# Kernel optimization log

Measured on AMD Instinct MI355X. Metric: run time of the kernel, lower is better.

The kernel has to match this reference:

```python
import jax, jax.numpy as jnp
import numpy as np

HIDDEN = 512
N_STEPS = 24
BATCH = 64
SEQ = 512
LN_EPS = 1e-5


def setup_inputs() -> dict:
    key = jax.random.key(0)
    ks = jax.random.split(key, 12)
    h = HIDDEN
    s = 0.05
    return {
        "enc_outputs": jax.random.normal(ks[0], (BATCH, SEQ, h), jnp.float32),
        "h_prev": jax.random.normal(ks[1], (1, BATCH, h), jnp.float32),
        # additive attention: score = v^T tanh(W_a [dec; enc] + b_a)
        "attn_We": jax.random.normal(ks[2], (h, h), jnp.float32) * s,   # enc half of W_a
        "attn_Wd": jax.random.normal(ks[3], (h, h), jnp.float32) * s,   # dec half of W_a
        "attn_b": jnp.zeros((h,), jnp.float32),
        "attn_v": jax.random.normal(ks[4], (h,), jnp.float32) * s,
        # GRU (PyTorch layout): W_ih (3h, 2h), W_hh (3h, h), gate order r,z,n
        "W_ih": jax.random.normal(ks[5], (3 * h, 2 * h), jnp.float32) * s,
        "W_hh": jax.random.normal(ks[6], (3 * h, h), jnp.float32) * s,
        "b_ih": jnp.zeros((3 * h,), jnp.float32),
        "b_hh": jnp.zeros((3 * h,), jnp.float32),
        # head: LayerNorm -> Linear(h, h//2) -> ReLU -> Linear(h//2, 1)
        "ln_g": jnp.ones((h,), jnp.float32),
        "ln_b": jnp.zeros((h,), jnp.float32),
        "W1": jax.random.normal(ks[7], (h, h // 2), jnp.float32) * s,
        "b1": jnp.zeros((h // 2,), jnp.float32),
        "W2": jax.random.normal(ks[8], (h // 2, 1), jnp.float32) * s,
        "b2": jnp.zeros((1,), jnp.float32),
    }


def _decode(enc_outputs, h0, attn_We, attn_Wd, attn_b, attn_v,
            W_ih, W_hh, b_ih, b_hh, ln_g, ln_b, W1, b1, W2, b2):
    H = enc_outputs.shape[-1]
    # encoder projection is loop-invariant: precompute once
    enc_proj = jnp.einsum("bse,eh->bsh", enc_outputs, attn_We)  # (B,S,H)

    def step(h, _):
        # h: (B, H) decoder state
        # additive attention
        q = h @ attn_Wd + attn_b                                  # (B,H)
        scores = jnp.einsum("bsh,h->bs", jnp.tanh(enc_proj + q[:, None, :]), attn_v)
        alpha = jax.nn.softmax(scores, axis=-1)                   # (B,S)
        context = jnp.einsum("bs,bsh->bh", alpha, enc_outputs)   # (B,H)
        # GRU cell on [context; state]
        x = jnp.concatenate([context, h], axis=-1)                # (B,2H)
        gi = x @ W_ih.T + b_ih                                    # (B,3H)
        gh = h @ W_hh.T + b_hh                                    # (B,3H)
        ir, iz, inn = jnp.split(gi, 3, axis=-1)
        hr, hz, hn = jnp.split(gh, 3, axis=-1)
        r = jax.nn.sigmoid(ir + hr)
        z = jax.nn.sigmoid(iz + hz)
        n = jnp.tanh(inn + r * hn)
        h_new = (1.0 - z) * n + z * h
        # head: LN -> Linear -> ReLU -> Linear
        mu = jnp.mean(h_new, axis=-1, keepdims=True)
        var = jnp.var(h_new, axis=-1, keepdims=True)
        y = (h_new - mu) * jax.lax.rsqrt(var + LN_EPS) * ln_g + ln_b
        y = jax.nn.relu(y @ W1 + b1)
        p = (y @ W2 + b2)[:, 0]                                   # (B,)
        return h_new, p

    h_final, preds = jax.lax.scan(step, h0, None, length=N_STEPS)
    preds = jnp.transpose(preds, (1, 0))[:, :, None]              # (B, n_steps, 1)
    return preds, h_final[None]                                   # (1,B,H)


def reference(enc_outputs, h_prev, attn_We, attn_Wd, attn_b, attn_v,
              W_ih, W_hh, b_ih, b_hh, ln_g, ln_b, W1, b1, W2, b2):
    return _decode(enc_outputs, h_prev[0], attn_We, attn_Wd, attn_b, attn_v,
                   W_ih, W_hh, b_ih, b_hh, ln_g, ln_b, W1, b1, W2, b2)
```

## Files before the change

### kernel.cpp

```cpp
#include <hip/hip_runtime.h>

typedef unsigned short u16;
typedef __attribute__((ext_vector_type(8))) short short8;
typedef __attribute__((ext_vector_type(4))) short short4v;
typedef __attribute__((ext_vector_type(4))) float f32x4;

#define NSTEP 24

__device__ __forceinline__ float b2f(u16 u){ return __uint_as_float(((unsigned)u)<<16); }
__device__ __forceinline__ u16 f2b(float f){
  unsigned u = __float_as_uint(f);
  u += 0x7fffu + ((u>>16)&1u);
  return (u16)(u>>16);
}
__device__ __forceinline__ float tanh_fast(float x){
  x = fminf(12.f, fmaxf(-12.f, x));
  float e = __expf(2.f*x);
  return __fdividef(e-1.f, e+1.f);
}
__device__ __forceinline__ float sigmoid_fast(float x){
  return __fdividef(1.f, 1.f + __expf(-x));
}

__global__ __launch_bounds__(256) void k_cvt(const float* __restrict__ in, u16* __restrict__ out, int n){
  int i = (blockIdx.x*256 + threadIdx.x)*4;
  if (i >= n) return;
  float4 v = *(const float4*)(in + i);
  short4v o;
  o[0] = (short)f2b(v.x); o[1] = (short)f2b(v.y); o[2] = (short)f2b(v.z); o[3] = (short)f2b(v.w);
  *(short4v*)(out + i) = o;
}

__global__ __launch_bounds__(256) void k_transpose512(const float* __restrict__ in, u16* __restrict__ out){
  __shared__ float tile[32][33];
  int tx = threadIdx.x, ty = threadIdx.y;
  int x = blockIdx.x*32 + tx;
  #pragma unroll
  for (int j=0;j<4;++j){
    int y = blockIdx.y*32 + ty + j*8;
    tile[ty+j*8][tx] = in[y*512 + x];
  }
  __syncthreads();
  int x2 = blockIdx.y*32 + tx;
  #pragma unroll
  for (int j=0;j<4;++j){
    int y2 = blockIdx.x*32 + ty + j*8;
    out[y2*512 + x2] = f2b(tile[tx][ty+j*8]);
  }
}

__global__ __launch_bounds__(256) void k_init(const float* __restrict__ h0, float* __restrict__ hf, u16* __restrict__ xcat){
  int idx = blockIdx.x*256 + threadIdx.x;
  float v = h0[idx];
  hf[idx] = v;
  xcat[(idx>>9)*1024 + 512 + (idx&511)] = f2b(v);
}

__global__ __launch_bounds__(256) void k_encproj(const u16* __restrict__ A, const u16* __restrict__ BT, u16* __restrict__ C){
  int w = threadIdx.x>>6, lane = threadIdx.x&63;
  int m0 = blockIdx.x*128 + (w>>1)*64;
  int n0 = blockIdx.y*128 + (w&1)*64;
  int r16 = lane&15, kof = (lane>>4)<<3;
  const u16* Ap = A + (m0+r16)*512 + kof;
  const u16* Bp = BT + (n0+r16)*512 + kof;
  f32x4 acc[4][4];
  #pragma unroll
  for (int i=0;i<4;++i)
    #pragma unroll
    for (int j=0;j<4;++j) acc[i][j] = (f32x4){0.f,0.f,0.f,0.f};
  #pragma unroll
  for (int k0=0;k0<512;k0+=32){
    short8 a[4], b[4];
    #pragma unroll
    for (int mf=0;mf<4;++mf) a[mf] = *(const short8*)(Ap + mf*16*512 + k0);
    #pragma unroll
    for (int nf=0;nf<4;++nf) b[nf] = *(const short8*)(Bp + nf*16*512 + k0);
    #pragma unroll
    for (int mf=0;mf<4;++mf)
      #pragma unroll
      for (int nf=0;nf<4;++nf)
        acc[mf][nf] = __builtin_amdgcn_mfma_f32_16x16x32_bf16(a[mf], b[nf], acc[mf][nf], 0,0,0);
  }
  int rb = (lane>>4)<<2;
  #pragma unroll
  for (int mf=0;mf<4;++mf)
    #pragma unroll
    for (int nf=0;nf<4;++nf)
      #pragma unroll
      for (int r=0;r<4;++r)
        C[(m0+mf*16+rb+r)*512 + n0+nf*16+r16] = f2b(acc[mf][nf][r]);
}

__device__ __forceinline__ void gemm_bt_core(const u16* A, int lda, const u16* BT, int ldb,
    const float* bias, float* C, int ldc, int K, int widx, bool accum){
  int lane = threadIdx.x & 63;
  int mt = widx & 3, nt = widx >> 2;
  int m0 = mt<<4, n0 = nt<<6;
  int r16 = lane&15, kof = (lane>>4)<<3;
  const u16* Ap = A + (m0+r16)*lda + kof;
  const u16* Bp = BT + (n0+r16)*ldb + kof;
  f32x4 acc[4];
  #pragma unroll
  for (int i=0;i<4;++i) acc[i] = (f32x4){0.f,0.f,0.f,0.f};
  #pragma unroll 4
  for (int k0=0;k0<K;k0+=32){
    short8 a = *(const short8*)(Ap + k0);
    #pragma unroll
    for (int nf=0;nf<4;++nf){
      short8 b = *(const short8*)(Bp + nf*16*ldb + k0);
      acc[nf] = __builtin_amdgcn_mfma_f32_16x16x32_bf16(a, b, acc[nf], 0,0,0);
    }
  }
  int rb = (lane>>4)<<2;
  #pragma unroll
  for (int nf=0;nf<4;++nf){
    int col = n0 + nf*16 + r16;
    float bv = bias ? bias[col] : 0.f;
    #pragma unroll
    for (int r=0;r<4;++r){
      float* p = &C[(m0+rb+r)*ldc + col];
      float v = acc[nf][r] + bv;
      if (accum) v += *p;
      *p = v;
    }
  }
}

__global__ __launch_bounds__(256) void k_sgh(const u16* __restrict__ ep, const float* __restrict__ q,
    const float* __restrict__ av, const u16* __restrict__ xcat,
    const u16* __restrict__ WhhB, const float* __restrict__ bhh,
    const u16* __restrict__ WihB, const float* __restrict__ bih,
    float* __restrict__ sc, float* __restrict__ gh, float* __restrict__ gi){
  int bid = blockIdx.x, tid = threadIdx.x;
  int wid = tid>>6, lane = tid&63;
  if (bid < 2048){
    int b = bid >> 5, sq = bid & 31;
    float qv[8], vv[8];
    {
      float4 q0 = *(const float4*)(q + b*512 + lane*8);
      float4 q1 = *(const float4*)(q + b*512 + lane*8 + 4);
      qv[0]=q0.x; qv[1]=q0.y; qv[2]=q0.z; qv[3]=q0.w;
      qv[4]=q1.x; qv[5]=q1.y; qv[6]=q1.z; qv[7]=q1.w;
      float4 v0 = *(const float4*)(av + lane*8);
      float4 v1 = *(const float4*)(av + lane*8 + 4);
      vv[0]=v0.x; vv[1]=v0.y; vv[2]=v0.z; vv[3]=v0.w;
      vv[4]=v1.x; vv[5]=v1.y; vv[6]=v1.z; vv[7]=v1.w;
    }
    int srow = sq*16 + wid*4;
    const u16* base = ep + (b*512 + srow)*512 + lane*8;
    short8 e0 = *(const short8*)(base);
    short8 e1 = *(const short8*)(base + 512);
    short8 e2 = *(const short8*)(base + 1024);
    short8 e3 = *(const short8*)(base + 1536);
    float r0=0.f, r1=0.f, r2=0.f, r3=0.f;
    #pragma unroll
    for (int j=0;j<8;++j){
      r0 += vv[j]*tanh_fast(b2f((u16)e0[j]) + qv[j]);
      r1 += vv[j]*tanh_fast(b2f((u16)e1[j]) + qv[j]);
      r2 += vv[j]*tanh_fast(b2f((u16)e2[j]) + qv[j]);
      r3 += vv[j]*tanh_fast(b2f((u16)e3[j]) + qv[j]);
    }
    #pragma unroll
    for (int off=32; off; off>>=1){
      r0 += __shfl_xor(r0, off);
      r1 += __shfl_xor(r1, off);
      r2 += __shfl_xor(r2, off);
      r3 += __shfl_xor(r3, off);
    }
    if (lane==0){
      sc[b*512 + srow]   = r0;
      sc[b*512 + srow+1] = r1;
      sc[b*512 + srow+2] = r2;
      sc[b*512 + srow+3] = r3;
    }
  } else if (bid < 2072){
    gemm_bt_core(xcat+512, 1024, WhhB, 512, bhh, gh, 1536, 512, (bid-2048)*4 + wid, false);
  } else {
    gemm_bt_core(xcat+512, 1024, WihB+512, 1024, bih, gi, 1536, 512, (bid-2072)*4 + wid, false);
  }
}

__global__ __launch_bounds__(256) void k_ctx(const float* __restrict__ sc, const u16* __restrict__ encB,
    u16* __restrict__ xcat){
  __shared__ float red[256];
  __shared__ float al[512];
  __shared__ float part[16][128];
  int t = threadIdx.x, hc = blockIdx.x, b = blockIdx.y;
  float s1 = sc[b*512 + t], s2 = sc[b*512 + 256 + t];
  red[t] = fmaxf(s1, s2); __syncthreads();
  for (int off=128; off; off>>=1){ if (t<off) red[t] = fmaxf(red[t], red[t+off]); __syncthreads(); }
  float mx = red[0]; __syncthreads();
  float e1 = __expf(s1-mx), e2 = __expf(s2-mx);
  red[t] = e1+e2; __syncthreads();
  for (int off=128; off; off>>=1){ if (t<off) red[t] += red[t+off]; __syncthreads(); }
  float inv = __fdividef(1.f, red[0]);
  al[t] = e1*inv; al[t+256] = e2*inv;
  __syncthreads();
  int cg = t & 15, sg = t >> 4;
  const u16* eb = encB + (b*512 + sg*32)*512 + hc*128 + cg*8;
  const float* alp = al + sg*32;
  float a8[8];
  #pragma unroll
  for (int j=0;j<8;++j) a8[j] = 0.f;
  #pragma unroll 8
  for (int s=0;s<32;++s){
    short8 e = *(const short8*)(eb + s*512);
    float a = alp[s];
    #pragma unroll
    for (int j=0;j<8;++j) a8[j] = fmaf(a, b2f((u16)e[j]), a8[j]);
  }
  #pragma unroll
  for (int j=0;j<8;++j) part[sg][cg*8+j] = a8[j];
  __syncthreads();
  if (t < 128){
    float v = 0.f;
    #pragma unroll
    for (int sg2=0;sg2<16;++sg2) v += part[sg2][t];
    xcat[b*1024 + hc*128 + t] = f2b(v);
  }
}

__global__ __launch_bounds__(256) void k_gictx(const u16* __restrict__ xcat, const u16* __restrict__ WihB,
    float* __restrict__ gi){
  int widx = blockIdx.x*4 + (threadIdx.x>>6);
  gemm_bt_core(xcat, 1024, WihB, 1024, (const float*)0, gi, 1536, 512, widx, true);
}

__device__ __forceinline__ void q_core(const float* hl, const u16* WdT, const float* ab, float* qrow){
  int tid = threadIdx.x;
  #pragma unroll
  for (int jj=0;jj<2;++jj){
    int j = tid + jj*256;
    float acc = ab[j];
    const u16* wr = WdT + j*512;
    #pragma unroll 4
    for (int k0=0;k0<512;k0+=8){
      short8 wv = *(const short8*)(wr + k0);
      #pragma unroll
      for (int i=0;i<8;++i) acc = fmaf(hl[k0+i], b2f((u16)wv[i]), acc);
    }
    qrow[j] = acc;
  }
}

__global__ __launch_bounds__(256) void k_q0(const float* __restrict__ hf, const u16* __restrict__ WdT,
    const float* __restrict__ ab, float* __restrict__ q){
  __shared__ float hl[512];
  int t = threadIdx.x, b = blockIdx.x;
  hl[t] = hf[b*512 + t];
  hl[t+256] = hf[b*512 + 256 + t];
  __syncthreads();
  q_core(hl, WdT, ab, q + b*512);
}

__global__ __launch_bounds__(256) void k_fin(const float* __restrict__ gi, const float* __restrict__ gh,
    const float* __restrict__ lng, const float* __restrict__ lnb,
    const float* __restrict__ W1, const float* __restrict__ b1,
    const float* __restrict__ W2, const float* __restrict__ b2,
    const u16* __restrict__ WdT, const float* __restrict__ ab,
    float* __restrict__ hf, u16* __restrict__ xcat, float* __restrict__ q,
    float* __restrict__ out, int step){
  __shared__ float hl[512];
  __shared__ float yn[512];
  __shared__ float red[256];
  int tid = threadIdx.x, b = blockIdx.x;
  #pragma unroll
  for (int jj=0;jj<2;++jj){
    int n = tid + jj*256;
    int gb = b*1536 + n;
    float r  = sigmoid_fast(gi[gb]      + gh[gb]);
    float z  = sigmoid_fast(gi[gb+512]  + gh[gb+512]);
    float nn = tanh_fast(gi[gb+1024] + r*gh[gb+1024]);
    float hp = hf[b*512 + n];
    float hnew = (1.f-z)*nn + z*hp;
    hf[b*512 + n] = hnew;
    xcat[b*1024 + 512 + n] = f2b(hnew);
    hl[n] = hnew;
    if (step == NSTEP-1) out[1536 + b*512 + n] = hnew;
  }
  __syncthreads();
  float h1 = hl[tid], h2 = hl[tid+256];
  red[tid] = h1+h2; __syncthreads();
  for (int off=128; off; off>>=1){ if (tid<off) red[tid]+=red[tid+off]; __syncthreads(); }
  float mu = red[0]*(1.f/512.f); __syncthreads();
  red[tid] = h1*h1+h2*h2; __syncthreads();
  for (int off=128; off; off>>=1){ if (tid<off) red[tid]+=red[tid+off]; __syncthreads(); }
  float var = red[0]*(1.f/512.f) - mu*mu; __syncthreads();
  float rs = rsqrtf(var + 1e-5f);
  yn[tid]     = (h1-mu)*rs*lng[tid] + lnb[tid];
  yn[tid+256] = (h2-mu)*rs*lng[tid+256] + lnb[tid+256];
  __syncthreads();
  float acc = b1[tid];
  #pragma unroll 8
  for (int k=0;k<512;++k) acc = fmaf(yn[k], W1[k*256+tid], acc);
  float y = fmaxf(acc, 0.f);
  red[tid] = y*W2[tid]; __syncthreads();
  for (int off=128; off; off>>=1){ if (tid<off) red[tid]+=red[tid+off]; __syncthreads(); }
  if (tid==0) out[b*24 + step] = red[0] + b2[0];
  if (step < NSTEP-1){
    __syncthreads();
    q_core(hl, WdT, ab, q + b*512);
  }
}

extern "C" void kernel_launch(void* const* d_in, const int* in_sizes, int n_in,
                              void* d_out, int out_size, void* d_ws, size_t ws_size,
                              hipStream_t stream){
  (void)in_sizes; (void)n_in; (void)out_size; (void)ws_size;
  const float* enc = (const float*)d_in[0];
  const float* h0  = (const float*)d_in[1];
  const float* We  = (const float*)d_in[2];
  const float* Wd  = (const float*)d_in[3];
  const float* ab  = (const float*)d_in[4];
  const float* av  = (const float*)d_in[5];
  const float* Wih = (const float*)d_in[6];
  const float* Whh = (const float*)d_in[7];
  const float* bih = (const float*)d_in[8];
  const float* bhh = (const float*)d_in[9];
  const float* lng = (const float*)d_in[10];
  const float* lnb = (const float*)d_in[11];
  const float* W1  = (const float*)d_in[12];
  const float* b1  = (const float*)d_in[13];
  const float* W2  = (const float*)d_in[14];
  const float* b2  = (const float*)d_in[15];
  float* out = (float*)d_out;
  char* ws = (char*)d_ws;
  u16*  ep   = (u16*)(ws + 0);
  u16*  encB = (u16*)(ws + 33554432);
  u16*  WeT  = (u16*)(ws + 67108864);
  u16*  WdT  = (u16*)(ws + 67633152);
  u16*  WihB = (u16*)(ws + 68157440);
  u16*  WhhB = (u16*)(ws + 71303168);
  float* hf  = (float*)(ws + 72876032);
  u16*  xcat = (u16*)(ws + 73007104);
  float* q   = (float*)(ws + 73138176);
  float* sc  = (float*)(ws + 73269248);
  float* gi  = (float*)(ws + 73400320);
  float* gh  = (float*)(ws + 73793536);

  k_cvt<<<16384, 256, 0, stream>>>(enc, encB, 16777216);
  k_cvt<<<1536, 256, 0, stream>>>(Wih, WihB, 1572864);
  k_cvt<<<768, 256, 0, stream>>>(Whh, WhhB, 786432);
  k_transpose512<<<dim3(16,16), dim3(32,8), 0, stream>>>(We, WeT);
  k_transpose512<<<dim3(16,16), dim3(32,8), 0, stream>>>(Wd, WdT);
  k_init<<<128, 256, 0, stream>>>(h0, hf, xcat);
  k_encproj<<<dim3(256,4), 256, 0, stream>>>(encB, WeT, ep);
  k_q0<<<64, 256, 0, stream>>>(hf, WdT, ab, q);
  for (int t=0; t<NSTEP; ++t){
    k_sgh<<<2096, 256, 0, stream>>>(ep, q, av, xcat, WhhB, bhh, WihB, bih, sc, gh, gi);
    k_ctx<<<dim3(4,64), 256, 0, stream>>>(sc, encB, xcat);
    k_gictx<<<24, 256, 0, stream>>>(xcat, WihB, gi);
    k_fin<<<64, 256, 0, stream>>>(gi, gh, lng, lnb, W1, b1, W2, b2, WdT, ab,
                                  hf, xcat, q, out, t);
  }
}
```

Before: 2.255 ms.

## Rebalance score and context kernels, move GRU hidden GEMMs beside context

The score kernel becomes a standalone 1024-block grid in which each wave handles 8 sequence rows instead of 4. The two h-dependent GEMMs (gh and the h half of gi) move out of the score launch and into the context kernel's launch. The context kernel now splits the hidden dimension into 8 chunks of 64 columns, giving 512 blocks instead of 256, which spreads the encoder read across more CUs. The cost is that each context block repeats the softmax reduction, and xcat is passed both read-only and writable, relying on the GEMMs reading only the h half while the context blocks write the other half.

```diff
diff --git a/kernel.cpp b/kernel.cpp
--- a/kernel.cpp
+++ b/kernel.cpp
@@ -126,97 +126,92 @@
   }
 }
 
-__global__ __launch_bounds__(256) void k_sgh(const u16* __restrict__ ep, const float* __restrict__ q,
-    const float* __restrict__ av, const u16* __restrict__ xcat,
+__global__ __launch_bounds__(256) void k_score(const u16* __restrict__ ep, const float* __restrict__ q,
+    const float* __restrict__ av, float* __restrict__ sc){
+  int b = blockIdx.y, sq = blockIdx.x;
+  int tid = threadIdx.x, wid = tid>>6, lane = tid&63;
+  float qv[8], vv[8];
+  {
+    float4 q0 = *(const float4*)(q + b*512 + lane*8);
+    float4 q1 = *(const float4*)(q + b*512 + lane*8 + 4);
+    qv[0]=q0.x; qv[1]=q0.y; qv[2]=q0.z; qv[3]=q0.w;
+    qv[4]=q1.x; qv[5]=q1.y; qv[6]=q1.z; qv[7]=q1.w;
+    float4 v0 = *(const float4*)(av + lane*8);
+    float4 v1 = *(const float4*)(av + lane*8 + 4);
+    vv[0]=v0.x; vv[1]=v0.y; vv[2]=v0.z; vv[3]=v0.w;
+    vv[4]=v1.x; vv[5]=v1.y; vv[6]=v1.z; vv[7]=v1.w;
+  }
+  int srow = sq*32 + wid*8;
+  const u16* base = ep + (b*512 + srow)*512 + lane*8;
+  short8 e[8];
+  #pragma unroll
+  for (int i=0;i<8;++i) e[i] = *(const short8*)(base + i*512);
+  float r[8];
+  #pragma unroll
+  for (int i=0;i<8;++i){
+    float acc = 0.f;
+    #pragma unroll
+    for (int j=0;j<8;++j)
+      acc += vv[j]*tanh_fast(b2f((u16)e[i][j]) + qv[j]);
+    r[i] = acc;
+  }
+  #pragma unroll
+  for (int off=32; off; off>>=1){
+    #pragma unroll
+    for (int i=0;i<8;++i) r[i] += __shfl_xor(r[i], off);
+  }
+  if (lane < 8) sc[b*512 + srow + lane] = r[lane];
+}
+
+__global__ __launch_bounds__(256) void k_cg(const float* __restrict__ sc, const u16* __restrict__ encB,
+    const u16* __restrict__ xcat_ro,
     const u16* __restrict__ WhhB, const float* __restrict__ bhh,
     const u16* __restrict__ WihB, const float* __restrict__ bih,
-    float* __restrict__ sc, float* __restrict__ gh, float* __restrict__ gi){
-  int bid = blockIdx.x, tid = threadIdx.x;
-  int wid = tid>>6, lane = tid&63;
-  if (bid < 2048){
-    int b = bid >> 5, sq = bid & 31;
-    float qv[8], vv[8];
-    {
-      float4 q0 = *(const float4*)(q + b*512 + lane*8);
-      float4 q1 = *(const float4*)(q + b*512 + lane*8 + 4);
-      qv[0]=q0.x; qv[1]=q0.y; qv[2]=q0.z; qv[3]=q0.w;
-      qv[4]=q1.x; qv[5]=q1.y; qv[6]=q1.z; qv[7]=q1.w;
-      float4 v0 = *(const float4*)(av + lane*8);
-      float4 v1 = *(const float4*)(av + lane*8 + 4);
-      vv[0]=v0.x; vv[1]=v0.y; vv[2]=v0.z; vv[3]=v0.w;
-      vv[4]=v1.x; vv[5]=v1.y; vv[6]=v1.z; vv[7]=v1.w;
-    }
-    int srow = sq*16 + wid*4;
-    const u16* base = ep + (b*512 + srow)*512 + lane*8;
-    short8 e0 = *(const short8*)(base);
-    short8 e1 = *(const short8*)(base + 512);
-    short8 e2 = *(const short8*)(base + 1024);
-    short8 e3 = *(const short8*)(base + 1536);
-    float r0=0.f, r1=0.f, r2=0.f, r3=0.f;
-    #pragma unroll
-    for (int j=0;j<8;++j){
-      r0 += vv[j]*tanh_fast(b2f((u16)e0[j]) + qv[j]);
-      r1 += vv[j]*tanh_fast(b2f((u16)e1[j]) + qv[j]);
-      r2 += vv[j]*tanh_fast(b2f((u16)e2[j]) + qv[j]);
-      r3 += vv[j]*tanh_fast(b2f((u16)e3[j]) + qv[j]);
-    }
-    #pragma unroll
-    for (int off=32; off; off>>=1){
-      r0 += __shfl_xor(r0, off);
-      r1 += __shfl_xor(r1, off);
-      r2 += __shfl_xor(r2, off);
-      r3 += __shfl_xor(r3, off);
-    }
-    if (lane==0){
-      sc[b*512 + srow]   = r0;
-      sc[b*512 + srow+1] = r1;
-      sc[b*512 + srow+2] = r2;
-      sc[b*512 + srow+3] = r3;
-    }
-  } else if (bid < 2072){
-    gemm_bt_core(xcat+512, 1024, WhhB, 512, bhh, gh, 1536, 512, (bid-2048)*4 + wid, false);
+    u16* __restrict__ xcat, float* __restrict__ gh, float* __restrict__ gi){
+  int bid = blockIdx.x, t = threadIdx.x;
+  if (bid < 512){
+    __shared__ float red[256];
+    __shared__ float al[512];
+    __shared__ float part[32][64];
+    int hc = bid & 7, b = bid >> 3;
+    float s1 = sc[b*512 + t], s2 = sc[b*512 + 256 + t];
+    red[t] = fmaxf(s1, s2); __syncthreads();
+    for (int off=128; off; off>>=1){ if (t<off) red[t] = fmaxf(red[t], red[t+off]); __syncthreads(); }
+    float mx = red[0]; __syncthreads();
+    float e1 = __expf(s1-mx), e2 = __expf(s2-mx);
+    red[t] = e1+e2; __syncthreads();
+    for (int off=128; off; off>>=1){ if (t<off) red[t] += red[t+off]; __syncthreads(); }
+    float inv = __fdividef(1.f, red[0]);
+    al[t] = e1*inv; al[t+256] = e2*inv;
+    __syncthreads();
+    int cg = t & 7, sg = t >> 3;
+    const u16* eb = encB + (b*512 + sg*16)*512 + hc*64 + cg*8;
+    const float* alp = al + sg*16;
+    float a8[8];
+    #pragma unroll
+    for (int j=0;j<8;++j) a8[j] = 0.f;
+    #pragma unroll
+    for (int s=0;s<16;++s){
+      short8 e = *(const short8*)(eb + s*512);
+      float a = alp[s];
+      #pragma unroll
+      for (int j=0;j<8;++j) a8[j] = fmaf(a, b2f((u16)e[j]), a8[j]);
+    }
+    #pragma unroll
+    for (int j=0;j<8;++j) part[sg][cg*8+j] = a8[j];
+    __syncthreads();
+    if (t < 64){
+      float v = 0.f;
+      #pragma unroll
+      for (int sg2=0;sg2<32;++sg2) v += part[sg2][t];
+      xcat[b*1024 + hc*64 + t] = f2b(v);
+    }
+  } else if (bid < 536){
+    int wid = t>>6;
+    gemm_bt_core(xcat_ro+512, 1024, WhhB, 512, bhh, gh, 1536, 512, (bid-512)*4 + wid, false);
   } else {
-    gemm_bt_core(xcat+512, 1024, WihB+512, 1024, bih, gi, 1536, 512, (bid-2072)*4 + wid, false);
-  }
-}
-
-__global__ __launch_bounds__(256) void k_ctx(const float* __restrict__ sc, const u16* __restrict__ encB,
-    u16* __restrict__ xcat){
-  __shared__ float red[256];
-  __shared__ float al[512];
-  __shared__ float part[16][128];
-  int t = threadIdx.x, hc = blockIdx.x, b = blockIdx.y;
-  float s1 = sc[b*512 + t], s2 = sc[b*512 + 256 + t];
-  red[t] = fmaxf(s1, s2); __syncthreads();
-  for (int off=128; off; off>>=1){ if (t<off) red[t] = fmaxf(red[t], red[t+off]); __syncthreads(); }
-  float mx = red[0]; __syncthreads();
-  float e1 = __expf(s1-mx), e2 = __expf(s2-mx);
-  red[t] = e1+e2; __syncthreads();
-  for (int off=128; off; off>>=1){ if (t<off) red[t] += red[t+off]; __syncthreads(); }
-  float inv = __fdividef(1.f, red[0]);
-  al[t] = e1*inv; al[t+256] = e2*inv;
-  __syncthreads();
-  int cg = t & 15, sg = t >> 4;
-  const u16* eb = encB + (b*512 + sg*32)*512 + hc*128 + cg*8;
-  const float* alp = al + sg*32;
-  float a8[8];
-  #pragma unroll
-  for (int j=0;j<8;++j) a8[j] = 0.f;
-  #pragma unroll 8
-  for (int s=0;s<32;++s){
-    short8 e = *(const short8*)(eb + s*512);
-    float a = alp[s];
-    #pragma unroll
-    for (int j=0;j<8;++j) a8[j] = fmaf(a, b2f((u16)e[j]), a8[j]);
-  }
-  #pragma unroll
-  for (int j=0;j<8;++j) part[sg][cg*8+j] = a8[j];
-  __syncthreads();
-  if (t < 128){
-    float v = 0.f;
-    #pragma unroll
-    for (int sg2=0;sg2<16;++sg2) v += part[sg2][t];
-    xcat[b*1024 + hc*128 + t] = f2b(v);
+    int wid = t>>6;
+    gemm_bt_core(xcat_ro+512, 1024, WihB+512, 1024, bih, gi, 1536, 512, (bid-536)*4 + wid, false);
   }
 }
 
@@ -347,8 +342,8 @@
   k_encproj<<<dim3(256,4), 256, 0, stream>>>(encB, WeT, ep);
   k_q0<<<64, 256, 0, stream>>>(hf, WdT, ab, q);
   for (int t=0; t<NSTEP; ++t){
-    k_sgh<<<2096, 256, 0, stream>>>(ep, q, av, xcat, WhhB, bhh, WihB, bih, sc, gh, gi);
-    k_ctx<<<dim3(4,64), 256, 0, stream>>>(sc, encB, xcat);
+    k_score<<<dim3(16,64), 256, 0, stream>>>(ep, q, av, sc);
+    k_cg<<<560, 256, 0, stream>>>(sc, encB, xcat, WhhB, bhh, WihB, bih, xcat, gh, gi);
     k_gictx<<<24, 256, 0, stream>>>(xcat, WihB, gi);
     k_fin<<<64, 256, 0, stream>>>(gi, gh, lng, lnb, W1, b1, W2, b2, WdT, ab,
                                   hf, xcat, q, out, t);
```

Measured after the change: 2.265 ms. Within noise of the previous version (+0.4%).
